# Kernel tuning notes

Hardware: AMD Instinct MI355X
Metric: run time of the kernel (lower is better)

## Reference

```python
import jax, jax.numpy as jnp
import numpy as np

G, T, D_IN, D_OUT = 8, 4096, 1024, 4096


def setup_inputs() -> dict:
    key = jax.random.key(0)
    k1, k2, k3 = jax.random.split(key, 3)
    x = jax.random.normal(k1, (T, D_IN), dtype=jnp.float32)
    # cumulative end offsets per group: sorted, last == T (grouped_mm convention)
    cuts = jnp.sort(jax.random.randint(k2, (G - 1,), 0, T, dtype=jnp.int32))
    offs = jnp.concatenate([cuts, jnp.array([T], dtype=jnp.int32)])
    weight = jax.random.normal(k3, (G, D_OUT, D_IN), dtype=jnp.float32) * (D_IN ** -0.5)
    return {"input": x, "grouped_mm_offs": offs, "weight": weight}


def reference(input, grouped_mm_offs, weight):
    # Grouped GEMM: row t (with offs[g-1] <= t < offs[g]) -> input[t] @ weight[g].T
    n_tok = input.shape[0]
    tok = jnp.arange(n_tok)
    gid = jnp.searchsorted(grouped_mm_offs, tok, side="right")  # [T] group id per row
    # Dense all-expert projection [G, T, D_OUT], then select the routed expert per row.
    proj = jnp.einsum("ti,goi->gto", input, weight)
    return proj[gid, tok]  # [T, D_OUT]
```

## Files before the change

### kernel.cpp

```cpp
#include <hip/hip_runtime.h>
#include <hip/hip_bf16.h>

#define NG 8
#define NT 4096
#define DIN 1024
#define DOUT 4096
#define BM 128
#define BN 128
#define BK 64
#define KTILES (DIN / BK)
#define TILESZ (BM * BK * 2)

typedef __attribute__((ext_vector_type(4))) float f32x4;
typedef __attribute__((ext_vector_type(8))) short bf16x8;

__device__ __forceinline__ int swz(int row, int colb) {
    return row * (BK * 2) + (colb ^ ((row & 7) << 4));
}

__device__ __forceinline__ unsigned long long pack4bf(f32x4 v) {
    union { __hip_bfloat16 h; unsigned short u; } c0, c1, c2, c3;
    c0.h = __float2bfloat16(v[0]);
    c1.h = __float2bfloat16(v[1]);
    c2.h = __float2bfloat16(v[2]);
    c3.h = __float2bfloat16(v[3]);
    return (unsigned long long)c0.u | ((unsigned long long)c1.u << 16) |
           ((unsigned long long)c2.u << 32) | ((unsigned long long)c3.u << 48);
}

__global__ __launch_bounds__(256, 2)
void grouped_gemm_bf16(const float* __restrict__ x,
                       const int* __restrict__ offs,
                       const float* __restrict__ w,
                       float* __restrict__ out) {
    __shared__ char lds[2 * TILESZ];
    char* lA = lds;
    char* lB = lds + TILESZ;

    const int rt = blockIdx.y;
    const int n0 = blockIdx.x * BN;
    int row0 = 0, endg = 0, gsel = -1;
    {
        int acc = 0, prev = 0;
        for (int g = 0; g < NG; ++g) {
            int e = offs[g];
            int cnt = (e - prev + BM - 1) / BM;
            if (rt < acc + cnt) { gsel = g; row0 = prev + (rt - acc) * BM; endg = e; break; }
            acc += cnt; prev = e;
        }
    }
    if (gsel < 0) return;
    const float* wg = w + (size_t)gsel * DOUT * DIN;

    const int tid  = threadIdx.x;
    const int lane = tid & 63;
    const int wid  = tid >> 6;
    const int wr   = wid >> 1, wc = wid & 1;
    const int lrow = lane & 15, kgrp = lane >> 4;
    const int sr   = tid >> 4;
    const int sc4  = tid & 15;

    int aoff[8], boff[8];
    #pragma unroll
    for (int i = 0; i < 8; ++i) {
        int r = sr + i * 16;
        int ar = row0 + r; if (ar >= endg) ar = endg - 1;
        aoff[i] = ar * DIN + sc4 * 4;
        boff[i] = (n0 + r) * DIN + sc4 * 4;
    }

    f32x4 acc[4][4];
    #pragma unroll
    for (int m = 0; m < 4; ++m)
        #pragma unroll
        for (int n = 0; n < 4; ++n)
            acc[m][n] = (f32x4){0.f, 0.f, 0.f, 0.f};

    f32x4 pA[8], pB[8];

    #pragma unroll
    for (int i = 0; i < 8; ++i) pA[i] = *(const f32x4*)(x + aoff[i]);
    #pragma unroll
    for (int i = 0; i < 8; ++i) pB[i] = *(const f32x4*)(wg + boff[i]);
    #pragma unroll
    for (int i = 0; i < 8; ++i)
        *(unsigned long long*)(lA + swz(sr + i * 16, sc4 * 8)) = pack4bf(pA[i]);
    #pragma unroll
    for (int i = 0; i < 8; ++i)
        *(unsigned long long*)(lB + swz(sr + i * 16, sc4 * 8)) = pack4bf(pB[i]);
    asm volatile("s_waitcnt lgkmcnt(0)" ::: "memory");
    __builtin_amdgcn_sched_barrier(0);
    __builtin_amdgcn_s_barrier();
    __builtin_amdgcn_sched_barrier(0);

    for (int kt = 0; kt < KTILES; ++kt) {
        if (kt + 1 < KTILES) {
            const int k0 = (kt + 1) * BK;
            #pragma unroll
            for (int i = 0; i < 8; ++i) pA[i] = *(const f32x4*)(x + aoff[i] + k0);
            #pragma unroll
            for (int i = 0; i < 8; ++i) pB[i] = *(const f32x4*)(wg + boff[i] + k0);
            __builtin_amdgcn_sched_barrier(0);
        }

        __builtin_amdgcn_s_setprio(1);
        #pragma unroll
        for (int kk = 0; kk < 2; ++kk) {
            const int kb = kk * 64 + kgrp * 16;
            bf16x8 af[4], bb[4];
            #pragma unroll
            for (int m = 0; m < 4; ++m)
                af[m] = *(const bf16x8*)(lA + swz(wr * 64 + m * 16 + lrow, kb));
            #pragma unroll
            for (int n = 0; n < 4; ++n)
                bb[n] = *(const bf16x8*)(lB + swz(wc * 64 + n * 16 + lrow, kb));
            #pragma unroll
            for (int m = 0; m < 4; ++m)
                #pragma unroll
                for (int n = 0; n < 4; ++n)
                    acc[m][n] = __builtin_amdgcn_mfma_f32_16x16x32_bf16(
                        af[m], bb[n], acc[m][n], 0, 0, 0);
        }
        __builtin_amdgcn_s_setprio(0);

        if (kt + 1 < KTILES) {
            __builtin_amdgcn_sched_barrier(0);
            __builtin_amdgcn_s_barrier();
            __builtin_amdgcn_sched_barrier(0);

            #pragma unroll
            for (int i = 0; i < 8; ++i)
                *(unsigned long long*)(lA + swz(sr + i * 16, sc4 * 8)) = pack4bf(pA[i]);
            #pragma unroll
            for (int i = 0; i < 8; ++i)
                *(unsigned long long*)(lB + swz(sr + i * 16, sc4 * 8)) = pack4bf(pB[i]);

            asm volatile("s_waitcnt lgkmcnt(0)" ::: "memory");
            __builtin_amdgcn_sched_barrier(0);
            __builtin_amdgcn_s_barrier();
            __builtin_amdgcn_sched_barrier(0);
        }
    }

    #pragma unroll
    for (int m = 0; m < 4; ++m) {
        #pragma unroll
        for (int j = 0; j < 4; ++j) {
            int row = row0 + wr * 64 + m * 16 + kgrp * 4 + j;
            if (row < endg) {
                #pragma unroll
                for (int n = 0; n < 4; ++n) {
                    int col = n0 + wc * 64 + n * 16 + lrow;
                    out[(size_t)row * DOUT + col] = acc[m][n][j];
                }
            }
        }
    }
}

extern "C" void kernel_launch(void* const* d_in, const int* in_sizes, int n_in,
                              void* d_out, int out_size, void* d_ws, size_t ws_size,
                              hipStream_t stream) {
    const float* x    = (const float*)d_in[0];
    const int*   offs = (const int*)d_in[1];
    const float* w    = (const float*)d_in[2];
    float* out = (float*)d_out;

    dim3 grid(DOUT / BN, NT / BM + NG, 1);
    grouped_gemm_bf16<<<grid, 256, 0, stream>>>(x, offs, w, out);
}
```

Before: 83.51 us.

## Pre-convert activations to bf16, enlarge M tile, and DMA A tiles to LDS

Adds a separate kernel that converts x to bf16 in workspace, so the GEMM loads A with global_load_lds directly into a double-buffered LDS region instead of converting in registers. The M tile doubles to 256, so each wave holds 8x4 accumulators and more A rows share each loaded weight tile. Weights are still converted from fp32 on the fly. This adds an extra kernel launch plus a round trip through memory for x, and raises register and LDS use, which may lower occupancy. Group-boundary tiles also waste more rows.

```diff
diff --git a/kernel.cpp b/kernel.cpp
--- a/kernel.cpp
+++ b/kernel.cpp
@@ -5,17 +5,22 @@
 #define NT 4096
 #define DIN 1024
 #define DOUT 4096
-#define BM 128
+#define BM 256
 #define BN 128
 #define BK 64
 #define KTILES (DIN / BK)
-#define TILESZ (BM * BK * 2)
+#define NTILES (DOUT / BN)
+#define RTILES (NT / BM + NG)
+#define ATILESZ (BM * BK * 2)
+#define BTILESZ (BN * BK * 2)
 
 typedef __attribute__((ext_vector_type(4))) float f32x4;
 typedef __attribute__((ext_vector_type(8))) short bf16x8;
 
-__device__ __forceinline__ int swz(int row, int colb) {
-    return row * (BK * 2) + (colb ^ ((row & 7) << 4));
+__device__ __forceinline__ void gld16(const void* g, void* l) {
+    __builtin_amdgcn_global_load_lds(
+        (const __attribute__((address_space(1))) void*)(g),
+        (__attribute__((address_space(3))) void*)(l), 16, 0, 0);
 }
 
 __device__ __forceinline__ unsigned long long pack4bf(f32x4 v) {
@@ -28,14 +33,27 @@
            ((unsigned long long)c2.u << 32) | ((unsigned long long)c3.u << 48);
 }
 
+__device__ __forceinline__ int swz(int row, int colb) {
+    return row * 128 + (colb ^ ((row & 7) << 4));
+}
+
+__global__ __launch_bounds__(256)
+void cvt_x_kernel(const float* __restrict__ x, short* __restrict__ xb) {
+    const int n4 = NT * DIN / 4;
+    for (int i = blockIdx.x * blockDim.x + threadIdx.x; i < n4;
+         i += gridDim.x * blockDim.x) {
+        f32x4 v = ((const f32x4*)x)[i];
+        ((unsigned long long*)xb)[i] = pack4bf(v);
+    }
+}
+
 __global__ __launch_bounds__(256, 2)
-void grouped_gemm_bf16(const float* __restrict__ x,
+void grouped_gemm_bf16(const short* __restrict__ xb,
                        const int* __restrict__ offs,
                        const float* __restrict__ w,
                        float* __restrict__ out) {
-    __shared__ char lds[2 * TILESZ];
-    char* lA = lds;
-    char* lB = lds + TILESZ;
+    __shared__ char lds[2 * ATILESZ + BTILESZ];
+    char* ldsB = lds + 2 * ATILESZ;
 
     const int rt = blockIdx.y;
     const int n0 = blockIdx.x * BN;
@@ -55,51 +73,56 @@
     const int tid  = threadIdx.x;
     const int lane = tid & 63;
     const int wid  = tid >> 6;
-    const int wr   = wid >> 1, wc = wid & 1;
+    const int wrM  = wid >> 1, wcN = wid & 1;
     const int lrow = lane & 15, kgrp = lane >> 4;
-    const int sr   = tid >> 4;
-    const int sc4  = tid & 15;
 
-    int aoff[8], boff[8];
+    int axoff[8], sbaseA[8];
     #pragma unroll
     for (int i = 0; i < 8; ++i) {
-        int r = sr + i * 16;
+        int stripe = i * 4 + wid;
+        int r = stripe * 8 + (lane >> 3);
+        int cs = (lane & 7) ^ (r & 7);
         int ar = row0 + r; if (ar >= endg) ar = endg - 1;
-        aoff[i] = ar * DIN + sc4 * 4;
-        boff[i] = (n0 + r) * DIN + sc4 * 4;
+        axoff[i]  = ar * DIN + cs * 8;
+        sbaseA[i] = stripe * 1024;
     }
+    const int sr = tid >> 4, sc4 = tid & 15;
+    int boff[8];
+    #pragma unroll
+    for (int i = 0; i < 8; ++i) boff[i] = (n0 + sr + i * 16) * DIN + sc4 * 4;
 
-    f32x4 acc[4][4];
+    f32x4 acc[8][4];
     #pragma unroll
-    for (int m = 0; m < 4; ++m)
+    for (int m = 0; m < 8; ++m)
         #pragma unroll
         for (int n = 0; n < 4; ++n)
             acc[m][n] = (f32x4){0.f, 0.f, 0.f, 0.f};
 
-    f32x4 pA[8], pB[8];
+    f32x4 pB[8];
 
     #pragma unroll
-    for (int i = 0; i < 8; ++i) pA[i] = *(const f32x4*)(x + aoff[i]);
+    for (int i = 0; i < 8; ++i) gld16(xb + axoff[i], lds + sbaseA[i]);
     #pragma unroll
     for (int i = 0; i < 8; ++i) pB[i] = *(const f32x4*)(wg + boff[i]);
     #pragma unroll
     for (int i = 0; i < 8; ++i)
-        *(unsigned long long*)(lA + swz(sr + i * 16, sc4 * 8)) = pack4bf(pA[i]);
-    #pragma unroll
-    for (int i = 0; i < 8; ++i)
-        *(unsigned long long*)(lB + swz(sr + i * 16, sc4 * 8)) = pack4bf(pB[i]);
-    asm volatile("s_waitcnt lgkmcnt(0)" ::: "memory");
+        *(unsigned long long*)(ldsB + swz(sr + i * 16, sc4 * 8)) = pack4bf(pB[i]);
+    asm volatile("s_waitcnt vmcnt(0) lgkmcnt(0)" ::: "memory");
     __builtin_amdgcn_sched_barrier(0);
     __builtin_amdgcn_s_barrier();
     __builtin_amdgcn_sched_barrier(0);
 
     for (int kt = 0; kt < KTILES; ++kt) {
+        const int cur = kt & 1;
+        const char* lA = lds + cur * ATILESZ;
+
         if (kt + 1 < KTILES) {
             const int k0 = (kt + 1) * BK;
             #pragma unroll
-            for (int i = 0; i < 8; ++i) pA[i] = *(const f32x4*)(x + aoff[i] + k0);
+            for (int i = 0; i < 8; ++i) pB[i] = *(const f32x4*)(wg + boff[i] + k0);
             #pragma unroll
-            for (int i = 0; i < 8; ++i) pB[i] = *(const f32x4*)(wg + boff[i] + k0);
+            for (int i = 0; i < 8; ++i)
+                gld16(xb + axoff[i] + k0, lds + (cur ^ 1) * ATILESZ + sbaseA[i]);
             __builtin_amdgcn_sched_barrier(0);
         }
 
@@ -107,15 +130,17 @@
         #pragma unroll
         for (int kk = 0; kk < 2; ++kk) {
             const int kb = kk * 64 + kgrp * 16;
-            bf16x8 af[4], bb[4];
+            bf16x8 af[8], bb[4];
             #pragma unroll
-            for (int m = 0; m < 4; ++m)
-                af[m] = *(const bf16x8*)(lA + swz(wr * 64 + m * 16 + lrow, kb));
+            for (int m = 0; m < 8; ++m) {
+                int r = wrM * 128 + m * 16 + lrow;
+                af[m] = *(const bf16x8*)(lA + r * 128 + (((kb >> 4) ^ (r & 7)) << 4));
+            }
             #pragma unroll
             for (int n = 0; n < 4; ++n)
-                bb[n] = *(const bf16x8*)(lB + swz(wc * 64 + n * 16 + lrow, kb));
+                bb[n] = *(const bf16x8*)(ldsB + swz(wcN * 64 + n * 16 + lrow, kb));
             #pragma unroll
-            for (int m = 0; m < 4; ++m)
+            for (int m = 0; m < 8; ++m)
                 #pragma unroll
                 for (int n = 0; n < 4; ++n)
                     acc[m][n] = __builtin_amdgcn_mfma_f32_16x16x32_bf16(
@@ -130,12 +155,9 @@
 
             #pragma unroll
             for (int i = 0; i < 8; ++i)
-                *(unsigned long long*)(lA + swz(sr + i * 16, sc4 * 8)) = pack4bf(pA[i]);
-            #pragma unroll
-            for (int i = 0; i < 8; ++i)
-                *(unsigned long long*)(lB + swz(sr + i * 16, sc4 * 8)) = pack4bf(pB[i]);
+                *(unsigned long long*)(ldsB + swz(sr + i * 16, sc4 * 8)) = pack4bf(pB[i]);
 
-            asm volatile("s_waitcnt lgkmcnt(0)" ::: "memory");
+            asm volatile("s_waitcnt vmcnt(0) lgkmcnt(0)" ::: "memory");
             __builtin_amdgcn_sched_barrier(0);
             __builtin_amdgcn_s_barrier();
             __builtin_amdgcn_sched_barrier(0);
@@ -143,14 +165,14 @@
     }
 
     #pragma unroll
-    for (int m = 0; m < 4; ++m) {
+    for (int m = 0; m < 8; ++m) {
         #pragma unroll
         for (int j = 0; j < 4; ++j) {
-            int row = row0 + wr * 64 + m * 16 + kgrp * 4 + j;
+            int row = row0 + wrM * 128 + m * 16 + kgrp * 4 + j;
             if (row < endg) {
                 #pragma unroll
                 for (int n = 0; n < 4; ++n) {
-                    int col = n0 + wc * 64 + n * 16 + lrow;
+                    int col = n0 + wcN * 64 + n * 16 + lrow;
                     out[(size_t)row * DOUT + col] = acc[m][n][j];
                 }
             }
@@ -165,7 +187,9 @@
     const int*   offs = (const int*)d_in[1];
     const float* w    = (const float*)d_in[2];
     float* out = (float*)d_out;
+    short* xb  = (short*)d_ws;
 
-    dim3 grid(DOUT / BN, NT / BM + NG, 1);
-    grouped_gemm_bf16<<<grid, 256, 0, stream>>>(x, offs, w, out);
+    cvt_x_kernel<<<1024, 256, 0, stream>>>(x, xb);
+    dim3 grid(NTILES, RTILES, 1);
+    grouped_gemm_bf16<<<grid, 256, 0, stream>>>(xb, offs, w, out);
 }
```

After: 81.51 us. 1.02x faster.
